# Optimization experiments

Hardware: AMD Instinct MI355X
Metric: run time of the kernel (lower is better)

The kernel has to match this reference:

```python
import jax, jax.numpy as jnp
import numpy as np

SEQ_LEN, BATCH, INPUT_SIZE, HIDDEN = 512, 64, 256, 512


def setup_inputs() -> dict:
    key = jax.random.key(0)
    ks = jax.random.split(key, 5)
    s_in = 1.0 / np.sqrt(INPUT_SIZE)
    s_h = 1.0 / np.sqrt(HIDDEN)
    x = jax.random.normal(ks[0], (SEQ_LEN, BATCH, INPUT_SIZE), dtype=jnp.float32)
    # gate order: f, i, o, c  (matches the torch module's lin_W*/lin_U*)
    Wx = jax.random.uniform(ks[1], (4, HIDDEN, INPUT_SIZE), jnp.float32, -s_in, s_in)
    bx = jax.random.uniform(ks[2], (4, HIDDEN), jnp.float32, -s_in, s_in)
    Wh = jax.random.uniform(ks[3], (4, HIDDEN, HIDDEN), jnp.float32, -s_h, s_h)
    bh = jax.random.uniform(ks[4], (4, HIDDEN), jnp.float32, -s_h, s_h)
    return {"x": x, "Wx": Wx, "bx": bx, "Wh": Wh, "bh": bh}


def reference(x, Wx, bx, Wh, bh):
    # x: [T, B, I]; Wx: [4, H, I]; Wh: [4, H, H]; biases: [4, H] (gate order f,i,o,c)
    T, B, _ = x.shape
    H = Wh.shape[-1]
    # Precompute input projections for all timesteps (batched GEMM): [T, 4, B, H]
    gx = jnp.einsum('tbi,ghi->tgbh', x, Wx) + bx[:, None, :]

    def step(carry, gx_t):
        h_prev, c_prev = carry
        gh = jnp.einsum('bh,gkh->gbk', h_prev, Wh) + bh[:, None, :]  # [4, B, H]
        g = gx_t + gh
        f = jax.nn.sigmoid(g[0])
        i = jax.nn.sigmoid(g[1])
        o = jax.nn.sigmoid(g[2])
        c = f * c_prev + i * jnp.tanh(g[3])
        h = o * jnp.tanh(c)
        return (h, c), h

    h0 = jnp.zeros((B, H), dtype=x.dtype)
    c0 = jnp.zeros((B, H), dtype=x.dtype)
    (h_last, c_last), h_seq = jax.lax.scan(step, (h0, c0), gx)
    return h_seq, h_last, c_last
```

## Files before the change

kernel.cpp:

```cpp
#include <hip/hip_runtime.h>
#include <hip/hip_cooperative_groups.h>
#include <math.h>

namespace cg = cooperative_groups;

#define TT 512
#define BB 64
#define II 256
#define HH 512

#define NTHREADS 512
#define NGRP 4
#define NCT  16
#define NBLOCKS (NGRP*NCT)

#define KPAD 776

typedef _Float16 f16x8 __attribute__((ext_vector_type(8)));
typedef _Float16 f16x4 __attribute__((ext_vector_type(4)));
typedef float    f32x4 __attribute__((ext_vector_type(4)));

__device__ __forceinline__ float sig_(float v)  { return 1.0f / (1.0f + __expf(-v)); }
__device__ __forceinline__ float tanh_(float v) { float e = __expf(2.0f * v); return 1.0f - 2.0f / (e + 1.0f); }

__device__ __forceinline__ void barrier_lds() {
    __builtin_amdgcn_sched_barrier(0);
    asm volatile("s_waitcnt lgkmcnt(0)" ::: "memory");
    __builtin_amdgcn_s_barrier();
    __builtin_amdgcn_sched_barrier(0);
}

__global__ void __launch_bounds__(NTHREADS, 2)
lstm_wflag(const float* __restrict__ x,
           const float* __restrict__ Wx,
           const float* __restrict__ bx,
           const float* __restrict__ Wh,
           const float* __restrict__ bh,
           float* __restrict__ out,
           unsigned int* __restrict__ flags,
           unsigned int* __restrict__ hbuf)
{
    __shared__ __align__(16) _Float16 AL[2][16 * KPAD];
    __shared__ __align__(16) float    exch[8 * 16 * 20];

    cg::grid_group grid = cg::this_grid();

    const int blk  = blockIdx.x;
    const int grp  = blk & 3;
    const int b0   = grp * 16;
    const int ct   = blk >> 2;
    const int hblk = ct * 32;

    const int tid = threadIdx.x;
    const int wv  = tid >> 6;
    const int L   = tid & 63;
    const int n   = L & 15;
    const int qd  = L >> 4;

    const int g  = n & 3;
    const int hu = hblk + wv * 4 + (n >> 2);
    f16x8 bfr[24];
    #pragma unroll
    for (int kc = 0; kc < 24; ++kc) {
        int k0 = kc * 32 + qd * 8;
        const float* src = (kc < 8)
            ? (Wx + ((size_t)g * HH + hu) * II + k0)
            : (Wh + ((size_t)g * HH + hu) * HH + (k0 - 256));
        float4 u0 = ((const float4*)src)[0];
        float4 u1 = ((const float4*)src)[1];
        f16x8 b = { (_Float16)u0.x, (_Float16)u0.y, (_Float16)u0.z, (_Float16)u0.w,
                    (_Float16)u1.x, (_Float16)u1.y, (_Float16)u1.z, (_Float16)u1.w };
        bfr[kc] = b;
    }

    const int be  = L >> 2;
    const int hle = L & 3;
    const int he  = hblk + wv * 4 + hle;
    float bias4[4];
    #pragma unroll
    for (int g2 = 0; g2 < 4; ++g2) bias4[g2] = bx[g2 * HH + he] + bh[g2 * HH + he];

    if (tid < 128)
        __hip_atomic_store(&flags[grp * 128 + tid], 0u,
                           __ATOMIC_RELAXED, __HIP_MEMORY_SCOPE_AGENT);
    grid.sync();

    const size_t HSEQ = (size_t)TT * BB * HH;
    float c_state = 0.0f;
    float* exchW = &exch[wv * 16 * 20];
    const int myflag = grp * 128 + ct * 8 + wv;

    for (int t = 0; t < TT; ++t) {
        const int p = t & 1;
        _Float16* ALp = AL[p];

        #pragma unroll
        for (int i = 0; i < 2; ++i) {
            int ch = tid + i * NTHREADS;
            int row = ch >> 6, pos = ch & 63;
            float4 v = ((const float4*)(x + ((size_t)t * BB + b0 + row) * II))[pos];
            f16x4 pk = { (_Float16)v.x, (_Float16)v.y, (_Float16)v.z, (_Float16)v.w };
            *(f16x4*)&ALp[row * KPAD + pos * 4] = pk;
        }

        if (t > 0) {
            const unsigned long long* fp =
                (const unsigned long long*)(flags + grp * 128);
            const unsigned tu = (unsigned)t;
            for (;;) {
                unsigned long long f2 = __hip_atomic_load(
                    &fp[L], __ATOMIC_RELAXED, __HIP_MEMORY_SCOPE_AGENT);
                unsigned lo = (unsigned)f2, hi = (unsigned)(f2 >> 32);
                if (__all((int)(lo >= tu && hi >= tu))) break;
                __builtin_amdgcn_s_sleep(1);
            }
            asm volatile("" ::: "memory");

            const unsigned long long* hsrc =
                (const unsigned long long*)(hbuf + (size_t)p * (BB * 256));
            #pragma unroll
            for (int i = 0; i < 4; ++i) {
                int ch = tid + i * NTHREADS;
                int row = ch >> 7, pos = ch & 127;
                unsigned long long u = __hip_atomic_load(
                    hsrc + (size_t)(b0 + row) * 128 + pos,
                    __ATOMIC_RELAXED, __HIP_MEMORY_SCOPE_AGENT);
                *(unsigned long long*)((char*)ALp + row * (KPAD * 2) + II * 2 + pos * 8) = u;
            }
        }

        barrier_lds();

        const char* Ab = (const char*)ALp + n * (KPAD * 2) + qd * 16;
        f32x4 a0 = { 0.f, 0.f, 0.f, 0.f };
        f32x4 a1 = { 0.f, 0.f, 0.f, 0.f };
        #pragma unroll
        for (int kc = 0; kc < 8; ++kc) {
            f16x8 a = *(const f16x8*)(Ab + kc * 64);
            if (kc & 1) a1 = __builtin_amdgcn_mfma_f32_16x16x32_f16(a, bfr[kc], a1, 0, 0, 0);
            else        a0 = __builtin_amdgcn_mfma_f32_16x16x32_f16(a, bfr[kc], a0, 0, 0, 0);
        }
        if (t > 0) {
            #pragma unroll
            for (int kc = 8; kc < 24; ++kc) {
                f16x8 a = *(const f16x8*)(Ab + kc * 64);
                if (kc & 1) a1 = __builtin_amdgcn_mfma_f32_16x16x32_f16(a, bfr[kc], a1, 0, 0, 0);
                else        a0 = __builtin_amdgcn_mfma_f32_16x16x32_f16(a, bfr[kc], a0, 0, 0, 0);
            }
        }
        f32x4 acc = a0 + a1;

        #pragma unroll
        for (int r = 0; r < 4; ++r)
            exchW[(qd * 4 + r) * 20 + n] = acc[r];
        float4 pre4 = *(const float4*)&exchW[be * 20 + hle * 4];

        float pf = pre4.x + bias4[0];
        float pi = pre4.y + bias4[1];
        float po = pre4.z + bias4[2];
        float pc = pre4.w + bias4[3];
        float fg = sig_(pf), ig = sig_(pi), og = sig_(po);
        float cn = fg * c_state + ig * tanh_(pc);
        float hv = og * tanh_(cn);
        c_state = cn;

        {
            union { _Float16 f; unsigned short u; } cv; cv.f = (_Float16)hv;
            unsigned mine  = cv.u;
            unsigned other = (unsigned)__shfl_xor((int)mine, 1, 64);
            if ((hle & 1) == 0) {
                unsigned pk = mine | (other << 16);
                unsigned int* hdst = hbuf + (size_t)((t + 1) & 1) * (BB * 256);
                __hip_atomic_store(&hdst[(unsigned)(b0 + be) * 256 + (unsigned)(he >> 1)],
                                   pk, __ATOMIC_RELAXED, __HIP_MEMORY_SCOPE_AGENT);
            }
        }

        __builtin_amdgcn_sched_barrier(0);
        asm volatile("s_waitcnt vmcnt(0)" ::: "memory");
        __builtin_amdgcn_sched_barrier(0);
        if (t != TT - 1 && L == 0)
            __hip_atomic_store(&flags[myflag], (unsigned)(t + 1),
                               __ATOMIC_RELAXED, __HIP_MEMORY_SCOPE_AGENT);

        out[((size_t)t * BB + b0 + be) * HH + he] = hv;
        if (t == TT - 1) {
            size_t r = (size_t)(b0 + be) * HH + he;
            out[HSEQ + r] = hv;
            out[HSEQ + (size_t)BB * HH + r] = cn;
        }
    }
}

extern "C" void kernel_launch(void* const* d_in, const int* in_sizes, int n_in,
                              void* d_out, int out_size, void* d_ws, size_t ws_size,
                              hipStream_t stream)
{
    const float* x  = (const float*)d_in[0];
    const float* Wx = (const float*)d_in[1];
    const float* bx = (const float*)d_in[2];
    const float* Wh = (const float*)d_in[3];
    const float* bh = (const float*)d_in[4];
    float* out = (float*)d_out;

    unsigned int* flags = (unsigned int*)d_ws;
    unsigned int* hbuf  = (unsigned int*)((char*)d_ws + 4096);

    void* args[] = { (void*)&x, (void*)&Wx, (void*)&bx, (void*)&bh,
                     (void*)&bh, (void*)&out, (void*)&flags, (void*)&hbuf };
    void* args2[] = { (void*)&x, (void*)&Wx, (void*)&bx, (void*)&Wh, (void*)&bh,
                      (void*)&out, (void*)&flags, (void*)&hbuf };
    (void)args;
    hipLaunchCooperativeKernel((const void*)lstm_wflag,
                               dim3(NBLOCKS), dim3(NTHREADS),
                               args2, 0, stream);
}
```

Measured before the change: 1.946 ms.

## Use per-block flags, swapped MFMA operands, and packed per-block h publication

Swaps the MFMA operands so each lane's accumulator holds all four gates for one (batch, hidden) pair, which removes the LDS exchange buffer. Hidden-state output is gathered in LDS and written to global memory by a single wave as contiguous per-block chunks, followed by one flag per block. Waiting now uses 16 flags per group, polled by one wave plus a block barrier, instead of 128 per-wave flags polled by every wave. The aim is to cut synchronisation traffic and latency on the per-step critical path, at the cost of an extra LDS barrier and a serialised single-wave publish.

After: 2.057 ms. 1.06x slower.

```diff
diff --git a/kernel.cpp b/kernel.cpp
--- a/kernel.cpp
+++ b/kernel.cpp
@@ -29,19 +29,26 @@
     __builtin_amdgcn_s_barrier();
     __builtin_amdgcn_sched_barrier(0);
 }
+__device__ __forceinline__ void barrier_raw() {
+    __builtin_amdgcn_sched_barrier(0);
+    asm volatile("" ::: "memory");
+    __builtin_amdgcn_s_barrier();
+    asm volatile("" ::: "memory");
+    __builtin_amdgcn_sched_barrier(0);
+}
 
 __global__ void __launch_bounds__(NTHREADS, 2)
-lstm_wflag(const float* __restrict__ x,
-           const float* __restrict__ Wx,
-           const float* __restrict__ bx,
-           const float* __restrict__ Wh,
-           const float* __restrict__ bh,
-           float* __restrict__ out,
-           unsigned int* __restrict__ flags,
-           unsigned int* __restrict__ hbuf)
+lstm_v4(const float* __restrict__ x,
+        const float* __restrict__ Wx,
+        const float* __restrict__ bx,
+        const float* __restrict__ Wh,
+        const float* __restrict__ bh,
+        float* __restrict__ out,
+        unsigned int* __restrict__ flags,
+        unsigned int* __restrict__ hbuf)
 {
     __shared__ __align__(16) _Float16 AL[2][16 * KPAD];
-    __shared__ __align__(16) float    exch[8 * 16 * 20];
+    __shared__ __align__(16) unsigned hvL[2][16][16];
 
     cg::grid_group grid = cg::this_grid();
 
@@ -57,38 +64,37 @@
     const int n   = L & 15;
     const int qd  = L >> 4;
 
-    const int g  = n & 3;
-    const int hu = hblk + wv * 4 + (n >> 2);
     f16x8 bfr[24];
-    #pragma unroll
-    for (int kc = 0; kc < 24; ++kc) {
-        int k0 = kc * 32 + qd * 8;
-        const float* src = (kc < 8)
-            ? (Wx + ((size_t)g * HH + hu) * II + k0)
-            : (Wh + ((size_t)g * HH + hu) * HH + (k0 - 256));
-        float4 u0 = ((const float4*)src)[0];
-        float4 u1 = ((const float4*)src)[1];
-        f16x8 b = { (_Float16)u0.x, (_Float16)u0.y, (_Float16)u0.z, (_Float16)u0.w,
-                    (_Float16)u1.x, (_Float16)u1.y, (_Float16)u1.z, (_Float16)u1.w };
-        bfr[kc] = b;
+    {
+        const int g  = n & 3;
+        const int hu = hblk + wv * 4 + (n >> 2);
+        #pragma unroll
+        for (int kc = 0; kc < 24; ++kc) {
+            int k0 = kc * 32 + qd * 8;
+            const float* src = (kc < 8)
+                ? (Wx + ((size_t)g * HH + hu) * II + k0)
+                : (Wh + ((size_t)g * HH + hu) * HH + (k0 - 256));
+            float4 u0 = ((const float4*)src)[0];
+            float4 u1 = ((const float4*)src)[1];
+            f16x8 b = { (_Float16)u0.x, (_Float16)u0.y, (_Float16)u0.z, (_Float16)u0.w,
+                        (_Float16)u1.x, (_Float16)u1.y, (_Float16)u1.z, (_Float16)u1.w };
+            bfr[kc] = b;
+        }
     }
 
-    const int be  = L >> 2;
-    const int hle = L & 3;
-    const int he  = hblk + wv * 4 + hle;
+    const int be = n;
+    const int he = hblk + wv * 4 + qd;
     float bias4[4];
     #pragma unroll
     for (int g2 = 0; g2 < 4; ++g2) bias4[g2] = bx[g2 * HH + he] + bh[g2 * HH + he];
 
-    if (tid < 128)
-        __hip_atomic_store(&flags[grp * 128 + tid], 0u,
+    if (tid == 0)
+        __hip_atomic_store(&flags[grp * 16 + ct], 0u,
                            __ATOMIC_RELAXED, __HIP_MEMORY_SCOPE_AGENT);
     grid.sync();
 
     const size_t HSEQ = (size_t)TT * BB * HH;
     float c_state = 0.0f;
-    float* exchW = &exch[wv * 16 * 20];
-    const int myflag = grp * 128 + ct * 8 + wv;
 
     for (int t = 0; t < TT; ++t) {
         const int p = t & 1;
@@ -104,84 +110,87 @@
         }
 
         if (t > 0) {
-            const unsigned long long* fp =
-                (const unsigned long long*)(flags + grp * 128);
-            const unsigned tu = (unsigned)t;
-            for (;;) {
-                unsigned long long f2 = __hip_atomic_load(
-                    &fp[L], __ATOMIC_RELAXED, __HIP_MEMORY_SCOPE_AGENT);
-                unsigned lo = (unsigned)f2, hi = (unsigned)(f2 >> 32);
-                if (__all((int)(lo >= tu && hi >= tu))) break;
-                __builtin_amdgcn_s_sleep(1);
-            }
-            asm volatile("" ::: "memory");
-
-            const unsigned long long* hsrc =
-                (const unsigned long long*)(hbuf + (size_t)p * (BB * 256));
+            if (wv == 0) {
+                const unsigned* fp = flags + grp * 16;
+                const unsigned tu = (unsigned)t;
+                for (;;) {
+                    unsigned f = (L < NCT)
+                        ? __hip_atomic_load(&fp[L], __ATOMIC_RELAXED, __HIP_MEMORY_SCOPE_AGENT)
+                        : 0xFFFFFFFFu;
+                    if (__all((int)(f >= tu))) break;
+                    __builtin_amdgcn_s_sleep(1);
+                }
+            }
+            barrier_raw();
+
+            const unsigned long long* hsrc = (const unsigned long long*)
+                (hbuf + ((size_t)p * NGRP + grp) * (NCT * 256));
             #pragma unroll
             for (int i = 0; i < 4; ++i) {
                 int ch = tid + i * NTHREADS;
-                int row = ch >> 7, pos = ch & 127;
+                int row = (ch >> 7) & 15;
+                int q   = ch & 127;
+                int j   = q >> 3, sub = q & 7;
                 unsigned long long u = __hip_atomic_load(
-                    hsrc + (size_t)(b0 + row) * 128 + pos,
+                    hsrc + (size_t)j * 128 + row * 8 + sub,
                     __ATOMIC_RELAXED, __HIP_MEMORY_SCOPE_AGENT);
-                *(unsigned long long*)((char*)ALp + row * (KPAD * 2) + II * 2 + pos * 8) = u;
+                *(unsigned long long*)((char*)ALp + row * (KPAD * 2) + II * 2 + j * 64 + sub * 8) = u;
             }
         }
 
         barrier_lds();
 
-        const char* Ab = (const char*)ALp + n * (KPAD * 2) + qd * 16;
+        const char* Bb = (const char*)ALp + n * (KPAD * 2) + qd * 16;
         f32x4 a0 = { 0.f, 0.f, 0.f, 0.f };
         f32x4 a1 = { 0.f, 0.f, 0.f, 0.f };
         #pragma unroll
         for (int kc = 0; kc < 8; ++kc) {
-            f16x8 a = *(const f16x8*)(Ab + kc * 64);
-            if (kc & 1) a1 = __builtin_amdgcn_mfma_f32_16x16x32_f16(a, bfr[kc], a1, 0, 0, 0);
-            else        a0 = __builtin_amdgcn_mfma_f32_16x16x32_f16(a, bfr[kc], a0, 0, 0, 0);
+            f16x8 bf = *(const f16x8*)(Bb + kc * 64);
+            if (kc & 1) a1 = __builtin_amdgcn_mfma_f32_16x16x32_f16(bfr[kc], bf, a1, 0, 0, 0);
+            else        a0 = __builtin_amdgcn_mfma_f32_16x16x32_f16(bfr[kc], bf, a0, 0, 0, 0);
         }
         if (t > 0) {
             #pragma unroll
             for (int kc = 8; kc < 24; ++kc) {
-                f16x8 a = *(const f16x8*)(Ab + kc * 64);
-                if (kc & 1) a1 = __builtin_amdgcn_mfma_f32_16x16x32_f16(a, bfr[kc], a1, 0, 0, 0);
-                else        a0 = __builtin_amdgcn_mfma_f32_16x16x32_f16(a, bfr[kc], a0, 0, 0, 0);
+                f16x8 bf = *(const f16x8*)(Bb + kc * 64);
+                if (kc & 1) a1 = __builtin_amdgcn_mfma_f32_16x16x32_f16(bfr[kc], bf, a1, 0, 0, 0);
+                else        a0 = __builtin_amdgcn_mfma_f32_16x16x32_f16(bfr[kc], bf, a0, 0, 0, 0);
             }
         }
         f32x4 acc = a0 + a1;
 
-        #pragma unroll
-        for (int r = 0; r < 4; ++r)
-            exchW[(qd * 4 + r) * 20 + n] = acc[r];
-        float4 pre4 = *(const float4*)&exchW[be * 20 + hle * 4];
-
-        float pf = pre4.x + bias4[0];
-        float pi = pre4.y + bias4[1];
-        float po = pre4.z + bias4[2];
-        float pc = pre4.w + bias4[3];
-        float fg = sig_(pf), ig = sig_(pi), og = sig_(po);
-        float cn = fg * c_state + ig * tanh_(pc);
+        float fg = sig_(acc[0] + bias4[0]);
+        float ig = sig_(acc[1] + bias4[1]);
+        float og = sig_(acc[2] + bias4[2]);
+        float cn = fg * c_state + ig * tanh_(acc[3] + bias4[3]);
         float hv = og * tanh_(cn);
         c_state = cn;
 
-        {
+        if (t != TT - 1) {
             union { _Float16 f; unsigned short u; } cv; cv.f = (_Float16)hv;
             unsigned mine  = cv.u;
-            unsigned other = (unsigned)__shfl_xor((int)mine, 1, 64);
-            if ((hle & 1) == 0) {
-                unsigned pk = mine | (other << 16);
-                unsigned int* hdst = hbuf + (size_t)((t + 1) & 1) * (BB * 256);
-                __hip_atomic_store(&hdst[(unsigned)(b0 + be) * 256 + (unsigned)(he >> 1)],
-                                   pk, __ATOMIC_RELAXED, __HIP_MEMORY_SCOPE_AGENT);
-            }
-        }
-
-        __builtin_amdgcn_sched_barrier(0);
-        asm volatile("s_waitcnt vmcnt(0)" ::: "memory");
-        __builtin_amdgcn_sched_barrier(0);
-        if (t != TT - 1 && L == 0)
-            __hip_atomic_store(&flags[myflag], (unsigned)(t + 1),
-                               __ATOMIC_RELAXED, __HIP_MEMORY_SCOPE_AGENT);
+            unsigned other = (unsigned)__shfl_xor((int)mine, 16, 64);
+            if ((qd & 1) == 0)
+                hvL[p][be][wv * 2 + (qd >> 1)] = mine | (other << 16);
+            barrier_lds();
+
+            if (wv == 7) {
+                const unsigned* s = &hvL[p][0][0];
+                uint4 v4 = *(const uint4*)(s + (L >> 2) * 16 + (L & 3) * 4);
+                unsigned long long w0 = (unsigned long long)v4.x | ((unsigned long long)v4.y << 32);
+                unsigned long long w1 = (unsigned long long)v4.z | ((unsigned long long)v4.w << 32);
+                unsigned long long* dst = (unsigned long long*)
+                    (hbuf + ((size_t)((t + 1) & 1) * NGRP + grp) * (NCT * 256) + ct * 256 + L * 4);
+                __hip_atomic_store(dst + 0, w0, __ATOMIC_RELAXED, __HIP_MEMORY_SCOPE_AGENT);
+                __hip_atomic_store(dst + 1, w1, __ATOMIC_RELAXED, __HIP_MEMORY_SCOPE_AGENT);
+                __builtin_amdgcn_sched_barrier(0);
+                asm volatile("s_waitcnt vmcnt(0)" ::: "memory");
+                __builtin_amdgcn_sched_barrier(0);
+                if (L == 0)
+                    __hip_atomic_store(&flags[grp * 16 + ct], (unsigned)(t + 1),
+                                       __ATOMIC_RELAXED, __HIP_MEMORY_SCOPE_AGENT);
+            }
+        }
 
         out[((size_t)t * BB + b0 + be) * HH + he] = hv;
         if (t == TT - 1) {
@@ -206,12 +215,9 @@
     unsigned int* flags = (unsigned int*)d_ws;
     unsigned int* hbuf  = (unsigned int*)((char*)d_ws + 4096);
 
-    void* args[] = { (void*)&x, (void*)&Wx, (void*)&bx, (void*)&bh,
-                     (void*)&bh, (void*)&out, (void*)&flags, (void*)&hbuf };
-    void* args2[] = { (void*)&x, (void*)&Wx, (void*)&bx, (void*)&Wh, (void*)&bh,
-                      (void*)&out, (void*)&flags, (void*)&hbuf };
-    (void)args;
-    hipLaunchCooperativeKernel((const void*)lstm_wflag,
+    void* args[] = { (void*)&x, (void*)&Wx, (void*)&bx, (void*)&Wh, (void*)&bh,
+                     (void*)&out, (void*)&flags, (void*)&hbuf };
+    hipLaunchCooperativeKernel((const void*)lstm_v4,
                                dim3(NBLOCKS), dim3(NTHREADS),
-                               args2, 0, stream);
-}
+                               args, 0, stream);
+}
```
